# Kernel tuning notes

Measured on AMD Instinct MI355X. Metric: run time of the kernel, lower is better.

Reference implementation:

```python
import jax, jax.numpy as jnp
import numpy as np

N_NODES = 100000
N_EDGES = 1600000
N_GRAPHS = 1000
H = 4

def _ln(x, g, b, eps=1e-5):
    m = x.mean(-1, keepdims=True)
    v = ((x - m) ** 2).mean(-1, keepdims=True)
    return (x - m) / jnp.sqrt(v + eps) * g + b

def _gat(x, src, dst, W, att_src, att_dst, bias, C):
    # PyG GATConv (self-loops already appended to src/dst): per-edge scores,
    # segment softmax over incoming edges of each dst node, scatter-add aggregation.
    N = x.shape[0]
    h = (x @ W.T).reshape(N, H, C)                      # [N,H,C]
    a_s = (h * att_src[None]).sum(-1)                   # [N,H]
    a_d = (h * att_dst[None]).sum(-1)                   # [N,H]
    e = jax.nn.leaky_relu(a_s[src] + a_d[dst], 0.2)     # [E,H]
    m = jax.ops.segment_max(e, dst, num_segments=N)
    w = jnp.exp(e - m[dst])
    denom = jax.ops.segment_sum(w, dst, num_segments=N)
    alpha = w / denom[dst]
    out = jax.ops.segment_sum(alpha[:, :, None] * h[src], dst, num_segments=N)
    return out.reshape(N, H * C) + bias

def _mha_len1(y, in_w, in_b, out_w, out_b, d):
    # seq_len==1 (x.unsqueeze(0)): softmax over a single key is identically 1,
    # so MHA(y,y,y) == out_proj(v_proj(y)). Exactly the original math.
    v = y @ in_w[2 * d:3 * d].T + in_b[2 * d:3 * d]
    return v @ out_w.T + out_b

def _forward(x, edge_index, batch, fc_feat_w, fc_feat_b,
             gat1_w, gat1_as, gat1_ad, gat1_b,
             gat2_w, gat2_as, gat2_ad, gat2_b,
             enc_in_w, enc_in_b, enc_out_w, enc_out_b,
             enc_f1_w, enc_f1_b, enc_f2_w, enc_f2_b,
             enc_ln1_g, enc_ln1_b, enc_ln2_g, enc_ln2_b,
             dec_sa_in_w, dec_sa_in_b, dec_sa_out_w, dec_sa_out_b,
             dec_ca_in_w, dec_ca_in_b, dec_ca_out_w, dec_ca_out_b,
             dec_f1_w, dec_f1_b, dec_f2_w, dec_f2_b,
             dec_ln1_g, dec_ln1_b, dec_ln2_g, dec_ln2_b, dec_ln3_g, dec_ln3_b,
             fc_w, fc_b):
    N = x.shape[0]
    d = 16 * H  # 64
    loop = jnp.arange(N, dtype=edge_index.dtype)
    src = jnp.concatenate([edge_index[0], loop])  # add_self_loops=True (PyG default)
    dst = jnp.concatenate([edge_index[1], loop])
    h = x @ fc_feat_w.T + fc_feat_b                     # feature_fc: [N,8]
    h = jax.nn.leaky_relu(_gat(h, src, dst, gat1_w, gat1_as, gat1_ad, gat1_b, 32), 0.01)
    h = jax.nn.leaky_relu(_gat(h, src, dst, gat2_w, gat2_as, gat2_ad, gat2_b, 16), 0.01)
    y = h  # [N,64]; transformer sees (L=1, B=N, E=64)
    for i in range(2):  # encoder layers
        a = _mha_len1(y, enc_in_w[i], enc_in_b[i], enc_out_w[i], enc_out_b[i], d)
        y = _ln(y + a, enc_ln1_g[i], enc_ln1_b[i])
        f = jax.nn.relu(y @ enc_f1_w[i].T + enc_f1_b[i]) @ enc_f2_w[i].T + enc_f2_b[i]
        y = _ln(y + f, enc_ln2_g[i], enc_ln2_b[i])
    for i in range(2):  # decoder layers (memory == tgt)
        a = _mha_len1(y, dec_sa_in_w[i], dec_sa_in_b[i], dec_sa_out_w[i], dec_sa_out_b[i], d)
        y = _ln(y + a, dec_ln1_g[i], dec_ln1_b[i])
        a = _mha_len1(y, dec_ca_in_w[i], dec_ca_in_b[i], dec_ca_out_w[i], dec_ca_out_b[i], d)
        y = _ln(y + a, dec_ln2_g[i], dec_ln2_b[i])
        f = jax.nn.relu(y @ dec_f1_w[i].T + dec_f1_b[i]) @ dec_f2_w[i].T + dec_f2_b[i]
        y = _ln(y + f, dec_ln3_g[i], dec_ln3_b[i])
    sums = jax.ops.segment_sum(y, batch, num_segments=N_GRAPHS)
    cnts = jax.ops.segment_sum(jnp.ones((N,), y.dtype), batch, num_segments=N_GRAPHS)
    pooled = sums / jnp.maximum(cnts, 1.0)[:, None]     # global_mean_pool
    return pooled @ fc_w.T + fc_b

def setup_inputs() -> dict:
    key = jax.random.key(0)
    ks = iter(jax.random.split(key, 64))
    p = lambda *s: jax.random.normal(next(ks), s, dtype=jnp.float32) * 0.1
    d = 64
    inp = {
        'x': jax.random.normal(next(ks), (N_NODES, 4), dtype=jnp.float32),
        'edge_index': jax.random.randint(next(ks), (2, N_EDGES), 0, N_NODES, dtype=jnp.int32),
        'batch': jnp.sort(jax.random.randint(next(ks), (N_NODES,), 0, N_GRAPHS, dtype=jnp.int32)),
        'fc_feat_w': p(8, 4), 'fc_feat_b': p(8),
        'gat1_w': p(128, 8), 'gat1_as': p(H, 32), 'gat1_ad': p(H, 32), 'gat1_b': p(128),
        'gat2_w': p(64, 128), 'gat2_as': p(H, 16), 'gat2_ad': p(H, 16), 'gat2_b': p(64),
        'enc_in_w': p(2, 3 * d, d), 'enc_in_b': p(2, 3 * d), 'enc_out_w': p(2, d, d), 'enc_out_b': p(2, d),
        'enc_f1_w': p(2, 256, d), 'enc_f1_b': p(2, 256), 'enc_f2_w': p(2, d, 256), 'enc_f2_b': p(2, d),
        'enc_ln1_g': jnp.ones((2, d)), 'enc_ln1_b': jnp.zeros((2, d)),
        'enc_ln2_g': jnp.ones((2, d)), 'enc_ln2_b': jnp.zeros((2, d)),
        'dec_sa_in_w': p(2, 3 * d, d), 'dec_sa_in_b': p(2, 3 * d), 'dec_sa_out_w': p(2, d, d), 'dec_sa_out_b': p(2, d),
        'dec_ca_in_w': p(2, 3 * d, d), 'dec_ca_in_b': p(2, 3 * d), 'dec_ca_out_w': p(2, d, d), 'dec_ca_out_b': p(2, d),
        'dec_f1_w': p(2, 256, d), 'dec_f1_b': p(2, 256), 'dec_f2_w': p(2, d, 256), 'dec_f2_b': p(2, d),
        'dec_ln1_g': jnp.ones((2, d)), 'dec_ln1_b': jnp.zeros((2, d)),
        'dec_ln2_g': jnp.ones((2, d)), 'dec_ln2_b': jnp.zeros((2, d)),
        'dec_ln3_g': jnp.ones((2, d)), 'dec_ln3_b': jnp.zeros((2, d)),
        'fc_w': p(33, d), 'fc_b': p(33),
    }
    return inp

def reference(x, edge_index, batch, fc_feat_w, fc_feat_b,
              gat1_w, gat1_as, gat1_ad, gat1_b,
              gat2_w, gat2_as, gat2_ad, gat2_b,
              enc_in_w, enc_in_b, enc_out_w, enc_out_b,
              enc_f1_w, enc_f1_b, enc_f2_w, enc_f2_b,
              enc_ln1_g, enc_ln1_b, enc_ln2_g, enc_ln2_b,
              dec_sa_in_w, dec_sa_in_b, dec_sa_out_w, dec_sa_out_b,
              dec_ca_in_w, dec_ca_in_b, dec_ca_out_w, dec_ca_out_b,
              dec_f1_w, dec_f1_b, dec_f2_w, dec_f2_b,
              dec_ln1_g, dec_ln1_b, dec_ln2_g, dec_ln2_b, dec_ln3_g, dec_ln3_b,
              fc_w, fc_b):
    return _forward(x, edge_index, batch, fc_feat_w, fc_feat_b,
                    gat1_w, gat1_as, gat1_ad, gat1_b,
                    gat2_w, gat2_as, gat2_ad, gat2_b,
                    enc_in_w, enc_in_b, enc_out_w, enc_out_b,
                    enc_f1_w, enc_f1_b, enc_f2_w, enc_f2_b,
                    enc_ln1_g, enc_ln1_b, enc_ln2_g, enc_ln2_b,
                    dec_sa_in_w, dec_sa_in_b, dec_sa_out_w, dec_sa_out_b,
                    dec_ca_in_w, dec_ca_in_b, dec_ca_out_w, dec_ca_out_b,
                    dec_f1_w, dec_f1_b, dec_f2_w, dec_f2_b,
                    dec_ln1_g, dec_ln1_b, dec_ln2_g, dec_ln2_b, dec_ln3_g, dec_ln3_b,
                    fc_w, fc_b)
```

## Files before the change

### kernel.cpp

```cpp
#include <hip/hip_runtime.h>

#define NN 100000
#define NE 1600000
#define NG 1000
#define ETOT (NE + NN)
#define NODES_PER_GRP 12500

typedef _Float16 f16x8 __attribute__((ext_vector_type(8)));
typedef _Float16 f16x4 __attribute__((ext_vector_type(4)));
typedef _Float16 f16x2 __attribute__((ext_vector_type(2)));
typedef float f32x16 __attribute__((ext_vector_type(16)));
#define XROW 72

__global__ void k_h1(const float* __restrict__ x, const float* __restrict__ ffw,
                     const float* __restrict__ ffb, const float* __restrict__ g1w,
                     const float* __restrict__ asw, const float* __restrict__ adw,
                     _Float16* __restrict__ h1p, float* __restrict__ asp,
                     float* __restrict__ ad_) {
    int tid = blockIdx.x * 256 + threadIdx.x;
    int n = __builtin_amdgcn_readfirstlane(tid >> 6);
    int jp = threadIdx.x & 63;
    float xv[4];
#pragma unroll
    for (int k = 0; k < 4; k++) xv[k] = x[n * 4 + k];
    float h0[8];
#pragma unroll
    for (int o = 0; o < 8; o++) {
        float a = ffb[o];
#pragma unroll
        for (int k = 0; k < 4; k++) a = fmaf(xv[k], ffw[o * 4 + k], a);
        h0[o] = a;
    }
    const float* w0 = g1w + jp * 8;
    const float* w1 = g1w + (jp + 64) * 8;
    float a0 = 0.f, a1 = 0.f;
#pragma unroll
    for (int k = 0; k < 8; k++) { a0 = fmaf(h0[k], w0[k], a0); a1 = fmaf(h0[k], w1[k], a1); }
    f16x2 r; r[0] = (_Float16)a0; r[1] = (_Float16)a1;
    *(f16x2*)(h1p + ((size_t)n * 64 + jp) * 2) = r;
    float p0 = a0 * asw[jp], p1 = a1 * asw[jp + 64];
    float d0 = a0 * adw[jp], d1 = a1 * adw[jp + 64];
#pragma unroll
    for (int m = 1; m <= 16; m <<= 1) {
        p0 += __shfl_xor(p0, m, 64); p1 += __shfl_xor(p1, m, 64);
        d0 += __shfl_xor(d0, m, 64); d1 += __shfl_xor(d1, m, 64);
    }
    if ((jp & 31) == 0) {
        int half = jp >> 5;
        *(float2*)(asp + n * 4 + half * 2) = make_float2(p0, p1);
        ad_[n * 4 + half] = d0;
        ad_[n * 4 + 2 + half] = d1;
    }
}

__global__ void k_att2(const _Float16* __restrict__ h2h, const float* __restrict__ asw,
                       const float* __restrict__ adw, float* __restrict__ as_,
                       float* __restrict__ ad_) {
    int tid = blockIdx.x * 256 + threadIdx.x;
    if (tid >= NN * 4) return;
    int n = tid >> 2, h = tid & 3;
    const _Float16* hp = h2h + (size_t)n * 64 + h * 16;
    const float* ws_ = asw + h * 16;
    const float* wd_ = adw + h * 16;
    float a = 0.f, d = 0.f;
#pragma unroll
    for (int c = 0; c < 16; c++) {
        float hv = (float)hp[c];
        a = fmaf(hv, ws_[c], a); d = fmaf(hv, wd_[c], d);
    }
    as_[tid] = a; ad_[tid] = d;
}

__global__ void k_count(const int* __restrict__ ei, int* __restrict__ deg) {
    int g = blockIdx.x & 7;
    int bi = blockIdx.x >> 3;
    int nb = gridDim.x >> 3;
    int lo = g * NODES_PER_GRP, hi = lo + NODES_PER_GRP;
    for (int e = bi * 256 + threadIdx.x; e < ETOT; e += nb * 256) {
        int dst = (e < NE) ? ei[NE + e] : (e - NE);
        if (dst >= lo && dst < hi) atomicAdd(&deg[dst], 1);
    }
}

__global__ void k_scan1(const int* __restrict__ deg, int* __restrict__ offs, int* __restrict__ bsum) {
    __shared__ int s[1024];
    int tid = threadIdx.x;
    int i = blockIdx.x * 1024 + tid;
    int v = (i < NN) ? deg[i] : 0;
    s[tid] = v;
    __syncthreads();
    for (int d = 1; d < 1024; d <<= 1) {
        int t = 0;
        if (tid >= d) t = s[tid - d];
        __syncthreads();
        if (tid >= d) s[tid] += t;
        __syncthreads();
    }
    if (i < NN) offs[i] = s[tid] - v;
    if (tid == 1023) bsum[blockIdx.x] = s[tid];
}

__global__ void k_scan2(int* __restrict__ bsum) {
    __shared__ int s[128];
    int tid = threadIdx.x;
    int v = (tid < 98) ? bsum[tid] : 0;
    s[tid] = v;
    __syncthreads();
    for (int d = 1; d < 128; d <<= 1) {
        int t = 0;
        if (tid >= d) t = s[tid - d];
        __syncthreads();
        if (tid >= d) s[tid] += t;
        __syncthreads();
    }
    bsum[tid] = s[tid] - v;
}

__global__ void k_scan3(int* __restrict__ offs, const int* __restrict__ bsum, int* __restrict__ cur) {
    int i = blockIdx.x * 1024 + threadIdx.x;
    if (i < NN) {
        int v = offs[i] + bsum[blockIdx.x];
        offs[i] = v; cur[i] = v;
    }
    if (i == 0) offs[NN] = ETOT;
}

__global__ void k_scatter(const int* __restrict__ ei, int* __restrict__ cur,
                          int* __restrict__ srcs, int* __restrict__ dsts) {
    int g = blockIdx.x & 7;
    int bi = blockIdx.x >> 3;
    int nb = gridDim.x >> 3;
    int lo = g * NODES_PER_GRP, hi = lo + NODES_PER_GRP;
    for (int e = bi * 256 + threadIdx.x; e < ETOT; e += nb * 256) {
        int dst = (e < NE) ? ei[NE + e] : (e - NE);
        if (dst >= lo && dst < hi) {
            int src = (e < NE) ? ei[e] : dst;
            int p = atomicAdd(&cur[dst], 1);
            srcs[p] = src;
            dsts[p] = dst;
        }
    }
}

__global__ void k_ew1(const int* __restrict__ srcs, const int* __restrict__ dsts,
                      const float* __restrict__ asp, const float* __restrict__ ad_,
                      uint2* __restrict__ ew) {
    int p = blockIdx.x * 256 + threadIdx.x;
    if (p >= ETOT) return;
    int s = srcs[p], d = dsts[p];
    float4 a = *(const float4*)(asp + s * 4);
    float4 b = *(const float4*)(ad_ + d * 4);
    float e0 = a.x + b.x; e0 = fmaxf(e0, 0.2f * e0);
    float e2 = a.y + b.z; e2 = fmaxf(e2, 0.2f * e2);
    float e1 = a.z + b.y; e1 = fmaxf(e1, 0.2f * e1);
    float e3 = a.w + b.w; e3 = fmaxf(e3, 0.2f * e3);
    union { unsigned u; _Float16 h[2]; } c0, c1;
    c0.h[0] = (_Float16)__expf(e0); c0.h[1] = (_Float16)__expf(e2);
    c1.h[0] = (_Float16)__expf(e1); c1.h[1] = (_Float16)__expf(e3);
    uint2 o; o.x = c0.u; o.y = c1.u;
    ew[p] = o;
}

__global__ void k_ew2(const int* __restrict__ srcs, const int* __restrict__ dsts,
                      const float* __restrict__ as_, const float* __restrict__ ad_,
                      uint2* __restrict__ ew) {
    int p = blockIdx.x * 256 + threadIdx.x;
    if (p >= ETOT) return;
    int s = srcs[p], d = dsts[p];
    float4 a = *(const float4*)(as_ + s * 4);
    float4 b = *(const float4*)(ad_ + d * 4);
    float e0 = a.x + b.x; e0 = fmaxf(e0, 0.2f * e0);
    float e1 = a.y + b.y; e1 = fmaxf(e1, 0.2f * e1);
    float e2 = a.z + b.z; e2 = fmaxf(e2, 0.2f * e2);
    float e3 = a.w + b.w; e3 = fmaxf(e3, 0.2f * e3);
    union { unsigned u; _Float16 h[2]; } c0, c1;
    c0.h[0] = (_Float16)__expf(e0); c0.h[1] = (_Float16)__expf(e1);
    c1.h[0] = (_Float16)__expf(e2); c1.h[1] = (_Float16)__expf(e3);
    uint2 o; o.x = c0.u; o.y = c1.u;
    ew[p] = o;
}

__global__ void k_gat1(const int* __restrict__ offs, const int* __restrict__ srcs,
                       const uint2* __restrict__ ew, const _Float16* __restrict__ h1p,
                       const float* __restrict__ bias, _Float16* __restrict__ g1h) {
    int wid = __builtin_amdgcn_readfirstlane((blockIdx.x * 256 + threadIdx.x) >> 6);
    int lane = threadIdx.x & 63;
    if (wid >= NN) return;
    int off = offs[wid];
    int deg = offs[wid + 1] - off;
    int hA = lane >> 5;
    float ws0 = 0.f, ws1 = 0.f, ac0 = 0.f, ac1 = 0.f;
    float ws0b = 0.f, ws1b = 0.f, ac0b = 0.f, ac1b = 0.f;
    for (int base = 0; base < deg; base += 64) {
        int idx = off + base + lane; if (idx >= ETOT) idx = ETOT - 1;
        int sv = srcs[idx];
        int cnt = deg - base; if (cnt > 64) cnt = 64;
        int j = 0;
        for (; j + 2 <= cnt; j += 2) {
            int sa = __builtin_amdgcn_readlane(sv, j);
            int sb = __builtin_amdgcn_readlane(sv, j + 1);
            uint2 wva = ew[off + base + j];
            uint2 wvb = ew[off + base + j + 1];
            f16x2 hpa = *(const f16x2*)(h1p + (size_t)sa * 128 + lane * 2);
            f16x2 hpb = *(const f16x2*)(h1p + (size_t)sb * 128 + lane * 2);
            union { unsigned u; _Float16 h[2]; } ca, cb;
            ca.u = hA ? wva.y : wva.x;
            cb.u = hA ? wvb.y : wvb.x;
            float w0 = (float)ca.h[0], w1 = (float)ca.h[1];
            float w0b = (float)cb.h[0], w1b = (float)cb.h[1];
            ws0 += w0; ws1 += w1;
            ac0 = fmaf(w0, (float)hpa[0], ac0); ac1 = fmaf(w1, (float)hpa[1], ac1);
            ws0b += w0b; ws1b += w1b;
            ac0b = fmaf(w0b, (float)hpb[0], ac0b); ac1b = fmaf(w1b, (float)hpb[1], ac1b);
        }
        if (j < cnt) {
            int sa = __builtin_amdgcn_readlane(sv, j);
            uint2 wva = ew[off + base + j];
            f16x2 hpa = *(const f16x2*)(h1p + (size_t)sa * 128 + lane * 2);
            union { unsigned u; _Float16 h[2]; } ca;
            ca.u = hA ? wva.y : wva.x;
            float w0 = (float)ca.h[0], w1 = (float)ca.h[1];
            ws0 += w0; ws1 += w1;
            ac0 = fmaf(w0, (float)hpa[0], ac0); ac1 = fmaf(w1, (float)hpa[1], ac1);
        }
    }
    ws0 += ws0b; ws1 += ws1b; ac0 += ac0b; ac1 += ac1b;
    float v0 = ac0 / ws0 + bias[lane];      v0 = fmaxf(v0, 0.01f * v0);
    float v1 = ac1 / ws1 + bias[lane + 64]; v1 = fmaxf(v1, 0.01f * v1);
    g1h[(size_t)wid * 128 + lane] = (_Float16)v0;
    g1h[(size_t)wid * 128 + lane + 64] = (_Float16)v1;
}

__global__ void k_gat2(const int* __restrict__ offs, const int* __restrict__ srcs,
                       const uint2* __restrict__ ew, const _Float16* __restrict__ h2h,
                       const float* __restrict__ bias, _Float16* __restrict__ g2h) {
    int wid = __builtin_amdgcn_readfirstlane((blockIdx.x * 256 + threadIdx.x) >> 6);
    int lane = threadIdx.x & 63;
    if (wid >= NN) return;
    int off = offs[wid];
    int deg = offs[wid + 1] - off;
    int hd = lane >> 4;
    float ws = 0.f, ac = 0.f, wsb = 0.f, acb = 0.f;
    for (int base = 0; base < deg; base += 64) {
        int idx = off + base + lane; if (idx >= ETOT) idx = ETOT - 1;
        int sv = srcs[idx];
        int cnt = deg - base; if (cnt > 64) cnt = 64;
        int j = 0;
        for (; j + 2 <= cnt; j += 2) {
            int sa = __builtin_amdgcn_readlane(sv, j);
            int sb = __builtin_amdgcn_readlane(sv, j + 1);
            uint2 wva = ew[off + base + j];
            uint2 wvb = ew[off + base + j + 1];
            float ha = (float)h2h[(size_t)sa * 64 + lane];
            float hb = (float)h2h[(size_t)sb * 64 + lane];
            unsigned sela = (hd & 2) ? wva.y : wva.x;
            unsigned selb = (hd & 2) ? wvb.y : wvb.x;
            union { unsigned u; _Float16 h[2]; } ca, cb;
            ca.u = (hd & 1) ? (sela >> 16) : sela;
            cb.u = (hd & 1) ? (selb >> 16) : selb;
            float wa = (float)ca.h[0], wb = (float)cb.h[0];
            ws += wa; ac = fmaf(wa, ha, ac);
            wsb += wb; acb = fmaf(wb, hb, acb);
        }
        if (j < cnt) {
            int sa = __builtin_amdgcn_readlane(sv, j);
            uint2 wva = ew[off + base + j];
            unsigned sela = (hd & 2) ? wva.y : wva.x;
            union { unsigned u; _Float16 h[2]; } ca;
            ca.u = (hd & 1) ? (sela >> 16) : sela;
            float wa = (float)ca.h[0];
            ws += wa; ac = fmaf(wa, (float)h2h[(size_t)sa * 64 + lane], ac);
        }
    }
    ws += wsb; ac += acb;
    float v = ac / ws + bias[lane]; v = fmaxf(v, 0.01f * v);
    g2h[(size_t)wid * 64 + lane] = (_Float16)v;
}

#define GROW 136
#define CROW 72
__global__ __launch_bounds__(256, 2) void k_h2m(const _Float16* __restrict__ g1h,
                                                const _Float16* __restrict__ apw2,
                                                _Float16* __restrict__ h2h) {
    __shared__ _Float16 ls[4 * 32 * GROW];
    const int t = threadIdx.x;
    const int w = t >> 6, l = t & 63;
    const int col = l & 31, hf = l >> 5;
    const int wv = blockIdx.x * 4 + w;
    const int nb = wv * 32;
    if (nb >= NN) return;
    _Float16* g16 = ls + w * (32 * GROW);
    const int r = l >> 1, hb = l & 1;
    {
        int nr = nb + r; if (nr >= NN) nr = NN - 1;
        const _Float16* src = g1h + (size_t)nr * 128 + hb * 64;
        _Float16* dst = g16 + r * GROW + hb * 64;
#pragma unroll
        for (int q = 0; q < 8; q++)
            *(f16x8*)(dst + q * 8) = *(const f16x8*)(src + q * 8);
    }
    f16x8 bf[8];
#pragma unroll
    for (int ks = 0; ks < 8; ks++)
        bf[ks] = *(const f16x8*)(g16 + col * GROW + ks * 16 + hf * 8);
    f32x16 acc0, acc1;
#pragma unroll
    for (int i = 0; i < 16; i++) { acc0[i] = 0.f; acc1[i] = 0.f; }
#pragma unroll
    for (int ks = 0; ks < 8; ks++) {
        f16x8 a0 = *(const f16x8*)(apw2 + ((0 * 8 + ks) * 64 + l) * 8);
        f16x8 a1 = *(const f16x8*)(apw2 + ((1 * 8 + ks) * 64 + l) * 8);
        acc0 = __builtin_amdgcn_mfma_f32_32x32x16_f16(a0, bf[ks], acc0, 0, 0, 0);
        acc1 = __builtin_amdgcn_mfma_f32_32x32x16_f16(a1, bf[ks], acc1, 0, 0, 0);
    }
    _Float16* c16 = g16;
#pragma unroll
    for (int rg = 0; rg < 4; rg++) {
        f16x4 h0, h1;
#pragma unroll
        for (int i = 0; i < 4; i++) { h0[i] = (_Float16)acc0[rg * 4 + i]; h1[i] = (_Float16)acc1[rg * 4 + i]; }
        *(f16x4*)(c16 + col * CROW + rg * 8 + hf * 4) = h0;
        *(f16x4*)(c16 + col * CROW + 32 + rg * 8 + hf * 4) = h1;
    }
    if (nb + r < NN) {
        _Float16* dst = h2h + (size_t)(nb + r) * 64 + hb * 32;
        const _Float16* srow = c16 + r * CROW + hb * 32;
#pragma unroll
        for (int q = 0; q < 4; q++)
            *(f16x8*)(dst + q * 8) = *(const f16x8*)(srow + q * 8);
    }
}

__global__ void k_fuse(const float* __restrict__ enc_in_w, const float* __restrict__ enc_in_b,
                       const float* __restrict__ enc_out_w, const float* __restrict__ enc_out_b,
                       const float* __restrict__ sa_in_w, const float* __restrict__ sa_in_b,
                       const float* __restrict__ sa_out_w, const float* __restrict__ sa_out_b,
                       const float* __restrict__ ca_in_w, const float* __restrict__ ca_in_b,
                       const float* __restrict__ ca_out_w, const float* __restrict__ ca_out_b,
                       _Float16* __restrict__ apk, float* __restrict__ fb) {
    int tid = blockIdx.x * 256 + threadIdx.x;
    int p = tid >> 12, r = tid & 4095, j = r >> 6, k = r & 63;
    int li = p & 1;
    const float *iw, *ib, *ow, *ob;
    if (p < 2)      { iw = enc_in_w + li * 12288; ib = enc_in_b + li * 192; ow = enc_out_w + li * 4096; ob = enc_out_b + li * 64; }
    else if (p < 4) { iw = sa_in_w + li * 12288;  ib = sa_in_b + li * 192;  ow = sa_out_w + li * 4096;  ob = sa_out_b + li * 64; }
    else            { iw = ca_in_w + li * 12288;  ib = ca_in_b + li * 192;  ow = ca_out_w + li * 4096;  ob = ca_out_b + li * 64; }
    float a = 0.f;
    for (int m = 0; m < 64; m++) a = fmaf(ow[j * 64 + m], iw[(128 + m) * 64 + k], a);
    int l = ((k >> 3) & 1) * 32 + (j & 31);
    apk[p * 4096 + (((j >> 5) * 4 + (k >> 4)) * 64 + l) * 8 + (k & 7)] = (_Float16)a;
    if (k == 0) {
        float fa = ob[j];
        for (int m = 0; m < 64; m++) fa = fmaf(ow[j * 64 + m], ib[128 + m], fa);
        fb[p * 64 + j] = fa;
// ... 242 lines not shown
        if (layer < 3) {
            xstore(xw, y, col, hf);
            loadbf(xw, bf, col, hf);
        }
    }
#pragma unroll
    for (int mt = 0; mt < 2; mt++)
#pragma unroll
        for (int nt = 0; nt < 2; nt++) {
            int n = nt ? nn1 : nn0;
            if (n < NN) {
                float* dst = yout + (size_t)n * 64 + mt * 32 + hf * 4;
#pragma unroll
                for (int rg = 0; rg < 4; rg++) {
                    const float* yp = &y[mt * 2 + nt][rg * 4];
                    *(float4*)(dst + rg * 8) = make_float4(yp[0], yp[1], yp[2], yp[3]);
                }
            }
        }
}

__global__ void k_pool(const float* __restrict__ y, const int* __restrict__ batch,
                       float* __restrict__ pooled) {
    int b = blockIdx.x;
    int t = threadIdx.x;
    int ch = t & 63, r = t >> 6;
    int lo = 0, hi = NN;
    while (lo < hi) { int mid = (lo + hi) >> 1; if (batch[mid] < b) lo = mid + 1; else hi = mid; }
    int st = lo;
    hi = NN;
    while (lo < hi) { int mid = (lo + hi) >> 1; if (batch[mid] < b + 1) lo = mid + 1; else hi = mid; }
    int en = lo;
    float s = 0.f;
    for (int i = st + r; i < en; i += 4) s += y[(size_t)i * 64 + ch];
    __shared__ float red[256];
    red[t] = s;
    __syncthreads();
    if (t < 64) {
        float tot = red[t] + red[t + 64] + red[t + 128] + red[t + 192];
        int cnt = en - st; if (cnt < 1) cnt = 1;
        pooled[b * 64 + t] = tot / (float)cnt;
    }
}

__global__ void k_fc(const float* __restrict__ pooled, const float* __restrict__ fcw,
                     const float* __restrict__ fcb, float* __restrict__ out) {
    int tid = blockIdx.x * 256 + threadIdx.x;
    if (tid >= NG * 33) return;
    int g = tid / 33, o = tid - g * 33;
    const float* p = pooled + g * 64;
    const float* w = fcw + o * 64;
    float a0 = 0.f, a1 = 0.f, a2 = 0.f, a3 = 0.f;
#pragma unroll
    for (int k = 0; k < 16; k++) {
        a0 = fmaf(p[4 * k], w[4 * k], a0);
        a1 = fmaf(p[4 * k + 1], w[4 * k + 1], a1);
        a2 = fmaf(p[4 * k + 2], w[4 * k + 2], a2);
        a3 = fmaf(p[4 * k + 3], w[4 * k + 3], a3);
    }
    out[tid] = fcb[o] + (a0 + a1) + (a2 + a3);
}

extern "C" void kernel_launch(void* const* d_in, const int* in_sizes, int n_in,
                              void* d_out, int out_size, void* d_ws, size_t ws_size,
                              hipStream_t stream) {
    (void)in_sizes; (void)n_in; (void)out_size; (void)ws_size;
    char* ws = (char*)d_ws;
    size_t o = 0;
    auto A = [&](size_t b) { size_t r = o; o += (b + 255) & ~(size_t)255; return r; };
    _Float16* h1p = (_Float16*)(ws + A((size_t)NN * 128 * 2));
    _Float16* h2h = (_Float16*)(ws + A((size_t)NN * 64 * 2));
    _Float16* g1h = (_Float16*)(ws + A((size_t)NN * 128 * 2));
    _Float16* g2h = (_Float16*)(ws + A((size_t)NN * 64 * 2));
    float* f_y   = (float*)(ws + A((size_t)NN * 64 * 4));
    float* f_asp = (float*)(ws + A((size_t)NN * 4 * 4));
    float* f_ad1 = (float*)(ws + A((size_t)NN * 4 * 4));
    float* f_as2 = (float*)(ws + A((size_t)NN * 4 * 4));
    float* f_ad2 = (float*)(ws + A((size_t)NN * 4 * 4));
    int* i_off   = (int*)(ws + A((size_t)(NN + 1) * 4));
    int* i_cur   = (int*)(ws + A((size_t)NN * 4));
    int* i_deg   = (int*)(ws + A((size_t)NN * 4));
    int* i_bsum  = (int*)(ws + A((size_t)1024 * 4));
    int* i_srcs  = (int*)(ws + A((size_t)ETOT * 4));
    int* i_dsts  = (int*)(ws + A((size_t)ETOT * 4));
    uint2* e_w   = (uint2*)(ws + A((size_t)ETOT * 8));
    float* f_fb  = (float*)(ws + A((size_t)6 * 64 * 4));
    _Float16* f_apk = (_Float16*)(ws + A((size_t)APK_TOT * 2));
    _Float16* apw2  = (_Float16*)(ws + A((size_t)8192 * 2));
    float* f_pool= (float*)(ws + A((size_t)NG * 64 * 4));

    const float* x   = (const float*)d_in[0];
    const int* ei    = (const int*)d_in[1];
    const int* batch = (const int*)d_in[2];
    #define F32(i) ((const float*)d_in[i])

    hipMemsetAsync(i_deg, 0, (size_t)NN * 4, stream);
    k_h1<<<NN * 64 / 256, 256, 0, stream>>>(x, F32(3), F32(4), F32(5), F32(6), F32(7),
                                            h1p, f_asp, f_ad1);
    k_count<<<8 * 128, 256, 0, stream>>>(ei, i_deg);
    k_scan1<<<98, 1024, 0, stream>>>(i_deg, i_off, i_bsum);
    k_scan2<<<1, 128, 0, stream>>>(i_bsum);
    k_scan3<<<98, 1024, 0, stream>>>(i_off, i_bsum, i_cur);
    k_scatter<<<8 * 128, 256, 0, stream>>>(ei, i_cur, i_srcs, i_dsts);
    k_ew1<<<(ETOT + 255) / 256, 256, 0, stream>>>(i_srcs, i_dsts, f_asp, f_ad1, e_w);
    k_gat1<<<NN * 64 / 256, 256, 0, stream>>>(i_off, i_srcs, e_w, h1p, F32(8), g1h);
    k_apack<<<544, 256, 0, stream>>>(F32(17), F32(33), F32(19), F32(35), F32(9), f_apk, apw2);
    k_h2m<<<(NN / 32 + 3) / 4, 256, 0, stream>>>(g1h, apw2, h2h);
    k_att2<<<(NN * 4 + 255) / 256, 256, 0, stream>>>(h2h, F32(10), F32(11), f_as2, f_ad2);
    k_ew2<<<(ETOT + 255) / 256, 256, 0, stream>>>(i_srcs, i_dsts, f_as2, f_ad2, e_w);
    k_gat2<<<NN * 64 / 256, 256, 0, stream>>>(i_off, i_srcs, e_w, h2h, F32(12), g2h);
    k_fuse<<<24576 / 256, 256, 0, stream>>>(F32(13), F32(14), F32(15), F32(16),
                                            F32(25), F32(26), F32(27), F32(28),
                                            F32(29), F32(30), F32(31), F32(32),
                                            f_apk, f_fb);
    XQ Q;
    Q.apk = f_apk; Q.fb = f_fb;
    Q.ef1b = F32(18); Q.ef2b = F32(20);
    Q.df1b = F32(34); Q.df2b = F32(36);
    Q.el1g = F32(21); Q.el1b = F32(22); Q.el2g = F32(23); Q.el2b = F32(24);
    Q.dl1g = F32(37); Q.dl1b = F32(38); Q.dl2g = F32(39); Q.dl2b = F32(40);
    Q.dl3g = F32(41); Q.dl3b = F32(42);
    k_xform<<<(NN + 255) / 256, 256, 0, stream>>>(g2h, f_y, Q);
    k_pool<<<NG, 256, 0, stream>>>(f_y, batch, f_pool);
    k_fc<<<(NG * 33 + 255) / 256, 256, 0, stream>>>(f_pool, F32(43), F32(44), (float*)d_out);
    #undef F32
}
```

Before: 597.5 us.

## Fuse edge-score computation into GAT aggregation and place self-loops via scan

```diff
diff --git a/kernel.cpp b/kernel.cpp
--- a/kernel.cpp
+++ b/kernel.cpp
@@ -11,6 +11,10 @@
 typedef _Float16 f16x2 __attribute__((ext_vector_type(2)));
 typedef float f32x16 __attribute__((ext_vector_type(16)));
 #define XROW 72
+
+__device__ __forceinline__ float rdlane_f(float v, int l) {
+    return __builtin_bit_cast(float, __builtin_amdgcn_readlane(__builtin_bit_cast(int, v), l));
+}
 
 __global__ void k_h1(const float* __restrict__ x, const float* __restrict__ ffw,
                      const float* __restrict__ ffb, const float* __restrict__ g1w,
@@ -76,8 +80,8 @@
     int bi = blockIdx.x >> 3;
     int nb = gridDim.x >> 3;
     int lo = g * NODES_PER_GRP, hi = lo + NODES_PER_GRP;
-    for (int e = bi * 256 + threadIdx.x; e < ETOT; e += nb * 256) {
-        int dst = (e < NE) ? ei[NE + e] : (e - NE);
+    for (int e = bi * 256 + threadIdx.x; e < NE; e += nb * 256) {
+        int dst = __builtin_nontemporal_load(ei + NE + e);
         if (dst >= lo && dst < hi) atomicAdd(&deg[dst], 1);
     }
 }
@@ -86,7 +90,7 @@
     __shared__ int s[1024];
     int tid = threadIdx.x;
     int i = blockIdx.x * 1024 + tid;
-    int v = (i < NN) ? deg[i] : 0;
+    int v = (i < NN) ? deg[i] + 1 : 0;
     s[tid] = v;
     __syncthreads();
     for (int d = 1; d < 1024; d <<= 1) {
@@ -116,72 +120,37 @@
     bsum[tid] = s[tid] - v;
 }
 
-__global__ void k_scan3(int* __restrict__ offs, const int* __restrict__ bsum, int* __restrict__ cur) {
+__global__ void k_scan3(int* __restrict__ offs, const int* __restrict__ bsum, int* __restrict__ cur,
+                        int* __restrict__ srcs) {
     int i = blockIdx.x * 1024 + threadIdx.x;
     if (i < NN) {
         int v = offs[i] + bsum[blockIdx.x];
-        offs[i] = v; cur[i] = v;
+        offs[i] = v;
+        cur[i] = v + 1;
+        srcs[v] = i;
     }
     if (i == 0) offs[NN] = ETOT;
 }
 
 __global__ void k_scatter(const int* __restrict__ ei, int* __restrict__ cur,
-                          int* __restrict__ srcs, int* __restrict__ dsts) {
+                          int* __restrict__ srcs) {
     int g = blockIdx.x & 7;
     int bi = blockIdx.x >> 3;
     int nb = gridDim.x >> 3;
     int lo = g * NODES_PER_GRP, hi = lo + NODES_PER_GRP;
-    for (int e = bi * 256 + threadIdx.x; e < ETOT; e += nb * 256) {
-        int dst = (e < NE) ? ei[NE + e] : (e - NE);
+    for (int e = bi * 256 + threadIdx.x; e < NE; e += nb * 256) {
+        int dst = __builtin_nontemporal_load(ei + NE + e);
         if (dst >= lo && dst < hi) {
-            int src = (e < NE) ? ei[e] : dst;
+            int src = __builtin_nontemporal_load(ei + e);
             int p = atomicAdd(&cur[dst], 1);
             srcs[p] = src;
-            dsts[p] = dst;
-        }
-    }
-}
-
-__global__ void k_ew1(const int* __restrict__ srcs, const int* __restrict__ dsts,
-                      const float* __restrict__ asp, const float* __restrict__ ad_,
-                      uint2* __restrict__ ew) {
-    int p = blockIdx.x * 256 + threadIdx.x;
-    if (p >= ETOT) return;
-    int s = srcs[p], d = dsts[p];
-    float4 a = *(const float4*)(asp + s * 4);
-    float4 b = *(const float4*)(ad_ + d * 4);
-    float e0 = a.x + b.x; e0 = fmaxf(e0, 0.2f * e0);
-    float e2 = a.y + b.z; e2 = fmaxf(e2, 0.2f * e2);
-    float e1 = a.z + b.y; e1 = fmaxf(e1, 0.2f * e1);
-    float e3 = a.w + b.w; e3 = fmaxf(e3, 0.2f * e3);
-    union { unsigned u; _Float16 h[2]; } c0, c1;
-    c0.h[0] = (_Float16)__expf(e0); c0.h[1] = (_Float16)__expf(e2);
-    c1.h[0] = (_Float16)__expf(e1); c1.h[1] = (_Float16)__expf(e3);
-    uint2 o; o.x = c0.u; o.y = c1.u;
-    ew[p] = o;
-}
-
-__global__ void k_ew2(const int* __restrict__ srcs, const int* __restrict__ dsts,
-                      const float* __restrict__ as_, const float* __restrict__ ad_,
-                      uint2* __restrict__ ew) {
-    int p = blockIdx.x * 256 + threadIdx.x;
-    if (p >= ETOT) return;
-    int s = srcs[p], d = dsts[p];
-    float4 a = *(const float4*)(as_ + s * 4);
-    float4 b = *(const float4*)(ad_ + d * 4);
-    float e0 = a.x + b.x; e0 = fmaxf(e0, 0.2f * e0);
-    float e1 = a.y + b.y; e1 = fmaxf(e1, 0.2f * e1);
-    float e2 = a.z + b.z; e2 = fmaxf(e2, 0.2f * e2);
-    float e3 = a.w + b.w; e3 = fmaxf(e3, 0.2f * e3);
-    union { unsigned u; _Float16 h[2]; } c0, c1;
-    c0.h[0] = (_Float16)__expf(e0); c0.h[1] = (_Float16)__expf(e1);
-    c1.h[0] = (_Float16)__expf(e2); c1.h[1] = (_Float16)__expf(e3);
-    uint2 o; o.x = c0.u; o.y = c1.u;
-    ew[p] = o;
+        }
+    }
 }
 
 __global__ void k_gat1(const int* __restrict__ offs, const int* __restrict__ srcs,
-                       const uint2* __restrict__ ew, const _Float16* __restrict__ h1p,
+                       const float* __restrict__ asp, const float* __restrict__ ad_,
+                       const _Float16* __restrict__ h1p,
                        const float* __restrict__ bias, _Float16* __restrict__ g1h) {
     int wid = __builtin_amdgcn_readfirstlane((blockIdx.x * 256 + threadIdx.x) >> 6);
     int lane = threadIdx.x & 63;
@@ -189,25 +158,32 @@
     int off = offs[wid];
     int deg = offs[wid + 1] - off;
     int hA = lane >> 5;
+    float4 bd = *(const float4*)(ad_ + wid * 4);
     float ws0 = 0.f, ws1 = 0.f, ac0 = 0.f, ac1 = 0.f;
     float ws0b = 0.f, ws1b = 0.f, ac0b = 0.f, ac1b = 0.f;
     for (int base = 0; base < deg; base += 64) {
         int idx = off + base + lane; if (idx >= ETOT) idx = ETOT - 1;
         int sv = srcs[idx];
+        float4 a = *(const float4*)(asp + sv * 4);
+        float e0 = a.x + bd.x; e0 = fmaxf(e0, 0.2f * e0);
+        float e2 = a.y + bd.z; e2 = fmaxf(e2, 0.2f * e2);
+        float e1 = a.z + bd.y; e1 = fmaxf(e1, 0.2f * e1);
+        float e3 = a.w + bd.w; e3 = fmaxf(e3, 0.2f * e3);
+        float wv0 = __expf(e0), wv1 = __expf(e1);
+        float wv2 = __expf(e2), wv3 = __expf(e3);
         int cnt = deg - base; if (cnt > 64) cnt = 64;
         int j = 0;
         for (; j + 2 <= cnt; j += 2) {
             int sa = __builtin_amdgcn_readlane(sv, j);
             int sb = __builtin_amdgcn_readlane(sv, j + 1);
-            uint2 wva = ew[off + base + j];
-            uint2 wvb = ew[off + base + j + 1];
             f16x2 hpa = *(const f16x2*)(h1p + (size_t)sa * 128 + lane * 2);
             f16x2 hpb = *(const f16x2*)(h1p + (size_t)sb * 128 + lane * 2);
-            union { unsigned u; _Float16 h[2]; } ca, cb;
-            ca.u = hA ? wva.y : wva.x;
-            cb.u = hA ? wvb.y : wvb.x;
-            float w0 = (float)ca.h[0], w1 = (float)ca.h[1];
-            float w0b = (float)cb.h[0], w1b = (float)cb.h[1];
+            float r0 = rdlane_f(wv0, j), r1 = rdlane_f(wv1, j);
+            float r2 = rdlane_f(wv2, j), r3 = rdlane_f(wv3, j);
+            float s0 = rdlane_f(wv0, j + 1), s1 = rdlane_f(wv1, j + 1);
+            float s2 = rdlane_f(wv2, j + 1), s3 = rdlane_f(wv3, j + 1);
+            float w0 = hA ? r1 : r0, w1 = hA ? r3 : r2;
+            float w0b = hA ? s1 : s0, w1b = hA ? s3 : s2;
             ws0 += w0; ws1 += w1;
             ac0 = fmaf(w0, (float)hpa[0], ac0); ac1 = fmaf(w1, (float)hpa[1], ac1);
             ws0b += w0b; ws1b += w1b;
@@ -215,11 +191,10 @@
         }
         if (j < cnt) {
             int sa = __builtin_amdgcn_readlane(sv, j);
-            uint2 wva = ew[off + base + j];
             f16x2 hpa = *(const f16x2*)(h1p + (size_t)sa * 128 + lane * 2);
-            union { unsigned u; _Float16 h[2]; } ca;
-            ca.u = hA ? wva.y : wva.x;
-            float w0 = (float)ca.h[0], w1 = (float)ca.h[1];
+            float r0 = rdlane_f(wv0, j), r1 = rdlane_f(wv1, j);
+            float r2 = rdlane_f(wv2, j), r3 = rdlane_f(wv3, j);
+            float w0 = hA ? r1 : r0, w1 = hA ? r3 : r2;
             ws0 += w0; ws1 += w1;
             ac0 = fmaf(w0, (float)hpa[0], ac0); ac1 = fmaf(w1, (float)hpa[1], ac1);
         }
@@ -232,7 +207,8 @@
 }
 
 __global__ void k_gat2(const int* __restrict__ offs, const int* __restrict__ srcs,
-                       const uint2* __restrict__ ew, const _Float16* __restrict__ h2h,
+                       const float* __restrict__ as_, const float* __restrict__ ad_,
+                       const _Float16* __restrict__ h2h,
                        const float* __restrict__ bias, _Float16* __restrict__ g2h) {
     int wid = __builtin_amdgcn_readfirstlane((blockIdx.x * 256 + threadIdx.x) >> 6);
     int lane = threadIdx.x & 63;
@@ -240,35 +216,42 @@
     int off = offs[wid];
     int deg = offs[wid + 1] - off;
     int hd = lane >> 4;
+    float4 bd = *(const float4*)(ad_ + wid * 4);
     float ws = 0.f, ac = 0.f, wsb = 0.f, acb = 0.f;
     for (int base = 0; base < deg; base += 64) {
         int idx = off + base + lane; if (idx >= ETOT) idx = ETOT - 1;
         int sv = srcs[idx];
+        float4 a = *(const float4*)(as_ + sv * 4);
+        float e0 = a.x + bd.x; e0 = fmaxf(e0, 0.2f * e0);
+        float e1 = a.y + bd.y; e1 = fmaxf(e1, 0.2f * e1);
+        float e2 = a.z + bd.z; e2 = fmaxf(e2, 0.2f * e2);
+        float e3 = a.w + bd.w; e3 = fmaxf(e3, 0.2f * e3);
+        float wv0 = __expf(e0), wv1 = __expf(e1);
+        float wv2 = __expf(e2), wv3 = __expf(e3);
         int cnt = deg - base; if (cnt > 64) cnt = 64;
         int j = 0;
         for (; j + 2 <= cnt; j += 2) {
             int sa = __builtin_amdgcn_readlane(sv, j);
             int sb = __builtin_amdgcn_readlane(sv, j + 1);
-            uint2 wva = ew[off + base + j];
-            uint2 wvb = ew[off + base + j + 1];
             float ha = (float)h2h[(size_t)sa * 64 + lane];
             float hb = (float)h2h[(size_t)sb * 64 + lane];
-            unsigned sela = (hd & 2) ? wva.y : wva.x;
-            unsigned selb = (hd & 2) ? wvb.y : wvb.x;
-            union { unsigned u; _Float16 h[2]; } ca, cb;
-            ca.u = (hd & 1) ? (sela >> 16) : sela;
-            cb.u = (hd & 1) ? (selb >> 16) : selb;
-            float wa = (float)ca.h[0], wb = (float)cb.h[0];
+            float r0 = rdlane_f(wv0, j), r1 = rdlane_f(wv1, j);
+            float r2 = rdlane_f(wv2, j), r3 = rdlane_f(wv3, j);
+            float s0 = rdlane_f(wv0, j + 1), s1 = rdlane_f(wv1, j + 1);
+            float s2 = rdlane_f(wv2, j + 1), s3 = rdlane_f(wv3, j + 1);
+            float t01 = (hd & 1) ? r1 : r0, t23 = (hd & 1) ? r3 : r2;
+            float wa = (hd & 2) ? t23 : t01;
+            float u01 = (hd & 1) ? s1 : s0, u23 = (hd & 1) ? s3 : s2;
+            float wb = (hd & 2) ? u23 : u01;
             ws += wa; ac = fmaf(wa, ha, ac);
             wsb += wb; acb = fmaf(wb, hb, acb);
         }
         if (j < cnt) {
             int sa = __builtin_amdgcn_readlane(sv, j);
-            uint2 wva = ew[off + base + j];
-            unsigned sela = (hd & 2) ? wva.y : wva.x;
-            union { unsigned u; _Float16 h[2]; } ca;
-            ca.u = (hd & 1) ? (sela >> 16) : sela;
-            float wa = (float)ca.h[0];
+            float r0 = rdlane_f(wv0, j), r1 = rdlane_f(wv1, j);
+            float r2 = rdlane_f(wv2, j), r3 = rdlane_f(wv3, j);
+            float t01 = (hd & 1) ? r1 : r0, t23 = (hd & 1) ? r3 : r2;
+            float wa = (hd & 2) ? t23 : t01;
             ws += wa; ac = fmaf(wa, (float)h2h[(size_t)sa * 64 + lane], ac);
         }
     }
@@ -678,8 +661,6 @@
     int* i_deg   = (int*)(ws + A((size_t)NN * 4));
     int* i_bsum  = (int*)(ws + A((size_t)1024 * 4));
     int* i_srcs  = (int*)(ws + A((size_t)ETOT * 4));
-    int* i_dsts  = (int*)(ws + A((size_t)ETOT * 4));
-    uint2* e_w   = (uint2*)(ws + A((size_t)ETOT * 8));
     float* f_fb  = (float*)(ws + A((size_t)6 * 64 * 4));
     _Float16* f_apk = (_Float16*)(ws + A((size_t)APK_TOT * 2));
     _Float16* apw2  = (_Float16*)(ws + A((size_t)8192 * 2));
@@ -696,15 +677,13 @@
     k_count<<<8 * 128, 256, 0, stream>>>(ei, i_deg);
     k_scan1<<<98, 1024, 0, stream>>>(i_deg, i_off, i_bsum);
     k_scan2<<<1, 128, 0, stream>>>(i_bsum);
-    k_scan3<<<98, 1024, 0, stream>>>(i_off, i_bsum, i_cur);
-    k_scatter<<<8 * 128, 256, 0, stream>>>(ei, i_cur, i_srcs, i_dsts);
-    k_ew1<<<(ETOT + 255) / 256, 256, 0, stream>>>(i_srcs, i_dsts, f_asp, f_ad1, e_w);
-    k_gat1<<<NN * 64 / 256, 256, 0, stream>>>(i_off, i_srcs, e_w, h1p, F32(8), g1h);
+    k_scan3<<<98, 1024, 0, stream>>>(i_off, i_bsum, i_cur, i_srcs);
+    k_scatter<<<8 * 128, 256, 0, stream>>>(ei, i_cur, i_srcs);
+    k_gat1<<<NN * 64 / 256, 256, 0, stream>>>(i_off, i_srcs, f_asp, f_ad1, h1p, F32(8), g1h);
     k_apack<<<544, 256, 0, stream>>>(F32(17), F32(33), F32(19), F32(35), F32(9), f_apk, apw2);
     k_h2m<<<(NN / 32 + 3) / 4, 256, 0, stream>>>(g1h, apw2, h2h);
     k_att2<<<(NN * 4 + 255) / 256, 256, 0, stream>>>(h2h, F32(10), F32(11), f_as2, f_ad2);
-    k_ew2<<<(ETOT + 255) / 256, 256, 0, stream>>>(i_srcs, i_dsts, f_as2, f_ad2, e_w);
-    k_gat2<<<NN * 64 / 256, 256, 0, stream>>>(i_off, i_srcs, e_w, h2h, F32(12), g2h);
+    k_gat2<<<NN * 64 / 256, 256, 0, stream>>>(i_off, i_srcs, f_as2, f_ad2, h2h, F32(12), g2h);
     k_fuse<<<24576 / 256, 256, 0, stream>>>(F32(13), F32(14), F32(15), F32(16),
                                             F32(25), F32(26), F32(27), F32(28),
                                             F32(29), F32(30), F32(31), F32(32),
```

Result: no change. 608.4 us (+1.8%).

## Drop dst array, place self-loops in scan, CSR-based edge weights, unrolled gathers

Applied to the files above, without the earlier changes.

```diff
diff --git a/kernel.cpp b/kernel.cpp
--- a/kernel.cpp
+++ b/kernel.cpp
@@ -76,8 +76,8 @@
     int bi = blockIdx.x >> 3;
     int nb = gridDim.x >> 3;
     int lo = g * NODES_PER_GRP, hi = lo + NODES_PER_GRP;
-    for (int e = bi * 256 + threadIdx.x; e < ETOT; e += nb * 256) {
-        int dst = (e < NE) ? ei[NE + e] : (e - NE);
+    for (int e = bi * 256 + threadIdx.x; e < NE; e += nb * 256) {
+        int dst = __builtin_nontemporal_load(ei + NE + e);
         if (dst >= lo && dst < hi) atomicAdd(&deg[dst], 1);
     }
 }
@@ -86,7 +86,7 @@
     __shared__ int s[1024];
     int tid = threadIdx.x;
     int i = blockIdx.x * 1024 + tid;
-    int v = (i < NN) ? deg[i] : 0;
+    int v = (i < NN) ? deg[i] + 1 : 0;
     s[tid] = v;
     __syncthreads();
     for (int d = 1; d < 1024; d <<= 1) {
@@ -116,68 +116,78 @@
     bsum[tid] = s[tid] - v;
 }
 
-__global__ void k_scan3(int* __restrict__ offs, const int* __restrict__ bsum, int* __restrict__ cur) {
+__global__ void k_scan3(int* __restrict__ offs, const int* __restrict__ bsum, int* __restrict__ cur,
+                        int* __restrict__ srcs) {
     int i = blockIdx.x * 1024 + threadIdx.x;
     if (i < NN) {
         int v = offs[i] + bsum[blockIdx.x];
-        offs[i] = v; cur[i] = v;
+        offs[i] = v;
+        cur[i] = v + 1;
+        srcs[v] = i;
     }
     if (i == 0) offs[NN] = ETOT;
 }
 
 __global__ void k_scatter(const int* __restrict__ ei, int* __restrict__ cur,
-                          int* __restrict__ srcs, int* __restrict__ dsts) {
+                          int* __restrict__ srcs) {
     int g = blockIdx.x & 7;
     int bi = blockIdx.x >> 3;
     int nb = gridDim.x >> 3;
     int lo = g * NODES_PER_GRP, hi = lo + NODES_PER_GRP;
-    for (int e = bi * 256 + threadIdx.x; e < ETOT; e += nb * 256) {
-        int dst = (e < NE) ? ei[NE + e] : (e - NE);
+    for (int e = bi * 256 + threadIdx.x; e < NE; e += nb * 256) {
+        int dst = __builtin_nontemporal_load(ei + NE + e);
         if (dst >= lo && dst < hi) {
-            int src = (e < NE) ? ei[e] : dst;
+            int src = __builtin_nontemporal_load(ei + e);
             int p = atomicAdd(&cur[dst], 1);
             srcs[p] = src;
-            dsts[p] = dst;
-        }
-    }
-}
-
-__global__ void k_ew1(const int* __restrict__ srcs, const int* __restrict__ dsts,
+        }
+    }
+}
+
+__global__ void k_ew1(const int* __restrict__ offs, const int* __restrict__ srcs,
                       const float* __restrict__ asp, const float* __restrict__ ad_,
                       uint2* __restrict__ ew) {
-    int p = blockIdx.x * 256 + threadIdx.x;
-    if (p >= ETOT) return;
-    int s = srcs[p], d = dsts[p];
-    float4 a = *(const float4*)(asp + s * 4);
+    int t = blockIdx.x * 256 + threadIdx.x;
+    int d = t >> 4, li = t & 15;
+    if (d >= NN) return;
+    int off = offs[d], deg = offs[d + 1] - off;
     float4 b = *(const float4*)(ad_ + d * 4);
-    float e0 = a.x + b.x; e0 = fmaxf(e0, 0.2f * e0);
-    float e2 = a.y + b.z; e2 = fmaxf(e2, 0.2f * e2);
-    float e1 = a.z + b.y; e1 = fmaxf(e1, 0.2f * e1);
-    float e3 = a.w + b.w; e3 = fmaxf(e3, 0.2f * e3);
-    union { unsigned u; _Float16 h[2]; } c0, c1;
-    c0.h[0] = (_Float16)__expf(e0); c0.h[1] = (_Float16)__expf(e2);
-    c1.h[0] = (_Float16)__expf(e1); c1.h[1] = (_Float16)__expf(e3);
-    uint2 o; o.x = c0.u; o.y = c1.u;
-    ew[p] = o;
-}
-
-__global__ void k_ew2(const int* __restrict__ srcs, const int* __restrict__ dsts,
+    for (int j = li; j < deg; j += 16) {
+        int s = srcs[off + j];
+        float4 a = *(const float4*)(asp + s * 4);
+        float e0 = a.x + b.x; e0 = fmaxf(e0, 0.2f * e0);
+        float e2 = a.y + b.z; e2 = fmaxf(e2, 0.2f * e2);
+        float e1 = a.z + b.y; e1 = fmaxf(e1, 0.2f * e1);
+        float e3 = a.w + b.w; e3 = fmaxf(e3, 0.2f * e3);
+        union { unsigned u; _Float16 h[2]; } c0, c1;
+        c0.h[0] = (_Float16)__expf(e0); c0.h[1] = (_Float16)__expf(e2);
+        c1.h[0] = (_Float16)__expf(e1); c1.h[1] = (_Float16)__expf(e3);
+        uint2 o; o.x = c0.u; o.y = c1.u;
+        ew[off + j] = o;
+    }
+}
+
+__global__ void k_ew2(const int* __restrict__ offs, const int* __restrict__ srcs,
                       const float* __restrict__ as_, const float* __restrict__ ad_,
                       uint2* __restrict__ ew) {
-    int p = blockIdx.x * 256 + threadIdx.x;
-    if (p >= ETOT) return;
-    int s = srcs[p], d = dsts[p];
-    float4 a = *(const float4*)(as_ + s * 4);
+    int t = blockIdx.x * 256 + threadIdx.x;
+    int d = t >> 4, li = t & 15;
+    if (d >= NN) return;
+    int off = offs[d], deg = offs[d + 1] - off;
     float4 b = *(const float4*)(ad_ + d * 4);
-    float e0 = a.x + b.x; e0 = fmaxf(e0, 0.2f * e0);
-    float e1 = a.y + b.y; e1 = fmaxf(e1, 0.2f * e1);
-    float e2 = a.z + b.z; e2 = fmaxf(e2, 0.2f * e2);
-    float e3 = a.w + b.w; e3 = fmaxf(e3, 0.2f * e3);
-    union { unsigned u; _Float16 h[2]; } c0, c1;
-    c0.h[0] = (_Float16)__expf(e0); c0.h[1] = (_Float16)__expf(e1);
-    c1.h[0] = (_Float16)__expf(e2); c1.h[1] = (_Float16)__expf(e3);
-    uint2 o; o.x = c0.u; o.y = c1.u;
-    ew[p] = o;
+    for (int j = li; j < deg; j += 16) {
+        int s = srcs[off + j];
+        float4 a = *(const float4*)(as_ + s * 4);
+        float e0 = a.x + b.x; e0 = fmaxf(e0, 0.2f * e0);
+        float e1 = a.y + b.y; e1 = fmaxf(e1, 0.2f * e1);
+        float e2 = a.z + b.z; e2 = fmaxf(e2, 0.2f * e2);
+        float e3 = a.w + b.w; e3 = fmaxf(e3, 0.2f * e3);
+        union { unsigned u; _Float16 h[2]; } c0, c1;
+        c0.h[0] = (_Float16)__expf(e0); c0.h[1] = (_Float16)__expf(e1);
+        c1.h[0] = (_Float16)__expf(e2); c1.h[1] = (_Float16)__expf(e3);
+        uint2 o; o.x = c0.u; o.y = c1.u;
+        ew[off + j] = o;
+    }
 }
 
 __global__ void k_gat1(const int* __restrict__ offs, const int* __restrict__ srcs,
@@ -189,39 +199,52 @@
     int off = offs[wid];
     int deg = offs[wid + 1] - off;
     int hA = lane >> 5;
+    const int* sp = srcs + off;
+    const uint2* wp = ew + off;
     float ws0 = 0.f, ws1 = 0.f, ac0 = 0.f, ac1 = 0.f;
     float ws0b = 0.f, ws1b = 0.f, ac0b = 0.f, ac1b = 0.f;
-    for (int base = 0; base < deg; base += 64) {
-        int idx = off + base + lane; if (idx >= ETOT) idx = ETOT - 1;
-        int sv = srcs[idx];
-        int cnt = deg - base; if (cnt > 64) cnt = 64;
-        int j = 0;
-        for (; j + 2 <= cnt; j += 2) {
-            int sa = __builtin_amdgcn_readlane(sv, j);
-            int sb = __builtin_amdgcn_readlane(sv, j + 1);
-            uint2 wva = ew[off + base + j];
-            uint2 wvb = ew[off + base + j + 1];
-            f16x2 hpa = *(const f16x2*)(h1p + (size_t)sa * 128 + lane * 2);
-            f16x2 hpb = *(const f16x2*)(h1p + (size_t)sb * 128 + lane * 2);
-            union { unsigned u; _Float16 h[2]; } ca, cb;
-            ca.u = hA ? wva.y : wva.x;
-            cb.u = hA ? wvb.y : wvb.x;
-            float w0 = (float)ca.h[0], w1 = (float)ca.h[1];
-            float w0b = (float)cb.h[0], w1b = (float)cb.h[1];
-            ws0 += w0; ws1 += w1;
-            ac0 = fmaf(w0, (float)hpa[0], ac0); ac1 = fmaf(w1, (float)hpa[1], ac1);
-            ws0b += w0b; ws1b += w1b;
-            ac0b = fmaf(w0b, (float)hpb[0], ac0b); ac1b = fmaf(w1b, (float)hpb[1], ac1b);
-        }
-        if (j < cnt) {
-            int sa = __builtin_amdgcn_readlane(sv, j);
-            uint2 wva = ew[off + base + j];
-            f16x2 hpa = *(const f16x2*)(h1p + (size_t)sa * 128 + lane * 2);
-            union { unsigned u; _Float16 h[2]; } ca;
-            ca.u = hA ? wva.y : wva.x;
-            float w0 = (float)ca.h[0], w1 = (float)ca.h[1];
-            ws0 += w0; ws1 += w1;
-            ac0 = fmaf(w0, (float)hpa[0], ac0); ac1 = fmaf(w1, (float)hpa[1], ac1);
+    int j = 0;
+    for (; j + 8 <= deg; j += 8) {
+        int sa[8]; uint2 wv[8];
+#pragma unroll
+        for (int q = 0; q < 8; q++) { sa[q] = sp[j + q]; wv[q] = wp[j + q]; }
+        f16x2 hp[8];
+#pragma unroll
+        for (int q = 0; q < 8; q++)
+            hp[q] = *(const f16x2*)(h1p + (size_t)sa[q] * 128 + lane * 2);
+#pragma unroll
+        for (int q = 0; q < 8; q++) {
+            union { unsigned u; _Float16 h[2]; } c;
+            c.u = hA ? wv[q].y : wv[q].x;
+            float w0 = (float)c.h[0], w1 = (float)c.h[1];
+            float h0v = (float)hp[q][0], h1v = (float)hp[q][1];
+            if (q & 1) { ws0b += w0; ws1b += w1; ac0b = fmaf(w0, h0v, ac0b); ac1b = fmaf(w1, h1v, ac1b); }
+            else       { ws0 += w0;  ws1 += w1;  ac0 = fmaf(w0, h0v, ac0);   ac1 = fmaf(w1, h1v, ac1); }
+        }
+    }
+    if (j < deg) {
+        int sa[8]; uint2 wv[8];
+#pragma unroll
+        for (int q = 0; q < 8; q++) {
+            int jj = j + q;
+            int jc = jj < deg ? jj : deg - 1;
+            sa[q] = sp[jc];
+            uint2 wt = wp[jc];
+            if (jj >= deg) { wt.x = 0u; wt.y = 0u; }
+            wv[q] = wt;
+        }
+        f16x2 hp[8];
+#pragma unroll
+        for (int q = 0; q < 8; q++)
+            hp[q] = *(const f16x2*)(h1p + (size_t)sa[q] * 128 + lane * 2);
+#pragma unroll
+        for (int q = 0; q < 8; q++) {
+            union { unsigned u; _Float16 h[2]; } c;
+            c.u = hA ? wv[q].y : wv[q].x;
+            float w0 = (float)c.h[0], w1 = (float)c.h[1];
+            float h0v = (float)hp[q][0], h1v = (float)hp[q][1];
+            if (q & 1) { ws0b += w0; ws1b += w1; ac0b = fmaf(w0, h0v, ac0b); ac1b = fmaf(w1, h1v, ac1b); }
+            else       { ws0 += w0;  ws1 += w1;  ac0 = fmaf(w0, h0v, ac0);   ac1 = fmaf(w1, h1v, ac1); }
         }
     }
     ws0 += ws0b; ws1 += ws1b; ac0 += ac0b; ac1 += ac1b;
@@ -240,36 +263,54 @@
     int off = offs[wid];
     int deg = offs[wid + 1] - off;
     int hd = lane >> 4;
+    int sh = (hd & 1) * 16;
+    const int* sp = srcs + off;
+    const uint2* wp = ew + off;
     float ws = 0.f, ac = 0.f, wsb = 0.f, acb = 0.f;
-    for (int base = 0; base < deg; base += 64) {
-        int idx = off + base + lane; if (idx >= ETOT) idx = ETOT - 1;
-        int sv = srcs[idx];
-        int cnt = deg - base; if (cnt > 64) cnt = 64;
-        int j = 0;
-        for (; j + 2 <= cnt; j += 2) {
-            int sa = __builtin_amdgcn_readlane(sv, j);
-            int sb = __builtin_amdgcn_readlane(sv, j + 1);
-            uint2 wva = ew[off + base + j];
-            uint2 wvb = ew[off + base + j + 1];
-            float ha = (float)h2h[(size_t)sa * 64 + lane];
-            float hb = (float)h2h[(size_t)sb * 64 + lane];
-            unsigned sela = (hd & 2) ? wva.y : wva.x;
-            unsigned selb = (hd & 2) ? wvb.y : wvb.x;
-            union { unsigned u; _Float16 h[2]; } ca, cb;
-            ca.u = (hd & 1) ? (sela >> 16) : sela;
-            cb.u = (hd & 1) ? (selb >> 16) : selb;
-            float wa = (float)ca.h[0], wb = (float)cb.h[0];
-            ws += wa; ac = fmaf(wa, ha, ac);
-            wsb += wb; acb = fmaf(wb, hb, acb);
-        }
-        if (j < cnt) {
-            int sa = __builtin_amdgcn_readlane(sv, j);
-            uint2 wva = ew[off + base + j];
-            unsigned sela = (hd & 2) ? wva.y : wva.x;
-            union { unsigned u; _Float16 h[2]; } ca;
-            ca.u = (hd & 1) ? (sela >> 16) : sela;
-            float wa = (float)ca.h[0];
-            ws += wa; ac = fmaf(wa, (float)h2h[(size_t)sa * 64 + lane], ac);
+    int j = 0;
+    for (; j + 8 <= deg; j += 8) {
+        int sa[8]; uint2 wv[8];
+#pragma unroll
+        for (int q = 0; q < 8; q++) { sa[q] = sp[j + q]; wv[q] = wp[j + q]; }
+        _Float16 hp[8];
+#pragma unroll
+        for (int q = 0; q < 8; q++)
+            hp[q] = h2h[(size_t)sa[q] * 64 + lane];
+#pragma unroll
+        for (int q = 0; q < 8; q++) {
+            unsigned sel = (hd & 2) ? wv[q].y : wv[q].x;
+            union { unsigned u; _Float16 h[2]; } c;
+            c.u = sel >> sh;
+            float w = (float)c.h[0];
+            float hv = (float)hp[q];
+            if (q & 1) { wsb += w; acb = fmaf(w, hv, acb); }
+            else       { ws += w;  ac = fmaf(w, hv, ac); }
+        }
+    }
+    if (j < deg) {
+        int sa[8]; uint2 wv[8];
+#pragma unroll
+        for (int q = 0; q < 8; q++) {
+            int jj = j + q;
+            int jc = jj < deg ? jj : deg - 1;
+            sa[q] = sp[jc];
+            uint2 wt = wp[jc];
+            if (jj >= deg) { wt.x = 0u; wt.y = 0u; }
+            wv[q] = wt;
+        }
+        _Float16 hp[8];
+#pragma unroll
+        for (int q = 0; q < 8; q++)
+            hp[q] = h2h[(size_t)sa[q] * 64 + lane];
+#pragma unroll
+        for (int q = 0; q < 8; q++) {
+            unsigned sel = (hd & 2) ? wv[q].y : wv[q].x;
+            union { unsigned u; _Float16 h[2]; } c;
+            c.u = sel >> sh;
+            float w = (float)c.h[0];
+            float hv = (float)hp[q];
+            if (q & 1) { wsb += w; acb = fmaf(w, hv, acb); }
+            else       { ws += w;  ac = fmaf(w, hv, ac); }
         }
     }
     ws += wsb; ac += acb;
@@ -678,7 +719,6 @@
     int* i_deg   = (int*)(ws + A((size_t)NN * 4));
     int* i_bsum  = (int*)(ws + A((size_t)1024 * 4));
     int* i_srcs  = (int*)(ws + A((size_t)ETOT * 4));
-    int* i_dsts  = (int*)(ws + A((size_t)ETOT * 4));
     uint2* e_w   = (uint2*)(ws + A((size_t)ETOT * 8));
     float* f_fb  = (float*)(ws + A((size_t)6 * 64 * 4));
     _Float16* f_apk = (_Float16*)(ws + A((size_t)APK_TOT * 2));
@@ -696,14 +736,14 @@
     k_count<<<8 * 128, 256, 0, stream>>>(ei, i_deg);
     k_scan1<<<98, 1024, 0, stream>>>(i_deg, i_off, i_bsum);
     k_scan2<<<1, 128, 0, stream>>>(i_bsum);
-    k_scan3<<<98, 1024, 0, stream>>>(i_off, i_bsum, i_cur);
-    k_scatter<<<8 * 128, 256, 0, stream>>>(ei, i_cur, i_srcs, i_dsts);
-    k_ew1<<<(ETOT + 255) / 256, 256, 0, stream>>>(i_srcs, i_dsts, f_asp, f_ad1, e_w);
+    k_scan3<<<98, 1024, 0, stream>>>(i_off, i_bsum, i_cur, i_srcs);
+    k_scatter<<<8 * 128, 256, 0, stream>>>(ei, i_cur, i_srcs);
+    k_ew1<<<NN * 16 / 256, 256, 0, stream>>>(i_off, i_srcs, f_asp, f_ad1, e_w);
     k_gat1<<<NN * 64 / 256, 256, 0, stream>>>(i_off, i_srcs, e_w, h1p, F32(8), g1h);
     k_apack<<<544, 256, 0, stream>>>(F32(17), F32(33), F32(19), F32(35), F32(9), f_apk, apw2);
     k_h2m<<<(NN / 32 + 3) / 4, 256, 0, stream>>>(g1h, apw2, h2h);
     k_att2<<<(NN * 4 + 255) / 256, 256, 0, stream>>>(h2h, F32(10), F32(11), f_as2, f_ad2);
-    k_ew2<<<(ETOT + 255) / 256, 256, 0, stream>>>(i_srcs, i_dsts, f_as2, f_ad2, e_w);
+    k_ew2<<<NN * 16 / 256, 256, 0, stream>>>(i_off, i_srcs, f_as2, f_ad2, e_w);
     k_gat2<<<NN * 64 / 256, 256, 0, stream>>>(i_off, i_srcs, e_w, h2h, F32(12), g2h);
     k_fuse<<<24576 / 256, 256, 0, stream>>>(F32(13), F32(14), F32(15), F32(16),
                                             F32(25), F32(26), F32(27), F32(28),
```

New measurement: 900.1 us. 50.6% more time.
